# Kernel optimization log

Hardware: AMD Instinct MI355X
Metric: run time of the kernel (lower is better)

The kernel has to match this reference:

```python
import jax, jax.numpy as jnp
import numpy as np

B, L, D = 64, 192, 1024        # batch, tokens (pre_len), in_dim
RES, DIFF, COND = 512, 256, 512
H, DH = 16, 64                 # heads, dim_head; inner = H*DH = 1024
INNER = H * DH
DFF = 4 * D                    # LinearEncoder d_ff
LC = 192                       # cond length


def setup_inputs() -> dict:
    key = jax.random.key(0)
    ks = jax.random.split(key, 16)
    n = lambda k, s, sc=1.0: jax.random.normal(k, s, dtype=jnp.float32) * sc
    return {
        "x": n(ks[0], (B, L, D)),
        "conds": n(ks[1], (B, LC, COND)),
        "diff_emb": n(ks[2], (B, DIFF)),
        "w_diff": n(ks[3], (2 * RES, DIFF), 0.02), "b_diff": jnp.zeros((2 * RES,), jnp.float32),
        "w_cond": n(ks[4], (2 * RES, COND), 0.02), "b_cond": jnp.zeros((2 * RES,), jnp.float32),
        "wq": n(ks[5], (INNER, D), 0.02),
        "wk": n(ks[6], (INNER, 2 * RES), 0.02),
        "wv": n(ks[7], (INNER, 2 * RES), 0.02),
        "wo": n(ks[8], (D, INNER), 0.02), "bo": jnp.zeros((D,), jnp.float32),
        "ln1_g": jnp.ones((D,), jnp.float32), "ln1_b": jnp.zeros((D,), jnp.float32),
        "ln2_g": jnp.ones((D,), jnp.float32), "ln2_b": jnp.zeros((D,), jnp.float32),
        "w_out": n(ks[9], (2 * D, RES), 0.02), "b_out": jnp.zeros((2 * D,), jnp.float32),
        "enc_wv": n(ks[10], (D, D), 0.02), "enc_bv": jnp.zeros((D,), jnp.float32),
        "enc_wo": n(ks[11], (D, D), 0.02), "enc_bo": jnp.zeros((D,), jnp.float32),
        "weight_mat": (jnp.eye(L, dtype=jnp.float32) + jax.random.normal(ks[12], (L, L), dtype=jnp.float32))[None],
        "conv1_w": n(ks[13], (DFF, D), 0.02), "conv1_b": jnp.zeros((DFF,), jnp.float32),
        "conv2_w": n(ks[14], (D, DFF), 0.02), "conv2_b": jnp.zeros((D,), jnp.float32),
        "enc_n1_g": jnp.ones((D,), jnp.float32), "enc_n1_b": jnp.zeros((D,), jnp.float32),
        "enc_n2_g": jnp.ones((D,), jnp.float32), "enc_n2_b": jnp.zeros((D,), jnp.float32),
    }


def _ln(x, g, b):
    m = jnp.mean(x, -1, keepdims=True)
    v = jnp.mean((x - m) ** 2, -1, keepdims=True)
    return (x - m) * jax.lax.rsqrt(v + 1e-5) * g + b


def reference(x, conds, diff_emb, w_diff, b_diff, w_cond, b_cond, wq, wk, wv, wo, bo,
              ln1_g, ln1_b, ln2_g, ln2_b, w_out, b_out, enc_wv, enc_bv, enc_wo, enc_bo,
              weight_mat, conv1_w, conv1_b, conv2_w, conv2_b,
              enc_n1_g, enc_n1_b, enc_n2_g, enc_n2_b):
    res = x
    # diff embedding broadcast-add (permute/unsqueeze in torch == add over token dim)
    x = x + (diff_emb @ w_diff.T + b_diff)[:, None, :]          # [B,L,D]
    # --- LinearEncoder (dropout is identity at inference) ---
    values = x @ enc_wv.T + enc_bv
    A = jax.nn.softplus(weight_mat[0])                          # [L,L]
    A = A / jnp.sum(A, -1, keepdims=True)                       # F.normalize(p=1)
    new_x = jnp.einsum('ij,bjd->bid', A, values)                # token mixing
    x = x + new_x @ enc_wo.T + enc_bo
    x = _ln(x, enc_n1_g, enc_n1_b)
    y = jax.nn.gelu(jnp.einsum('bld,fd->blf', x, conv1_w) + conv1_b, approximate=False)
    y = jnp.einsum('blf,df->bld', y, conv2_w) + conv2_b
    x = _ln(x + y, enc_n2_g, enc_n2_b)
    # --- norm1 + cross attention ---
    x = _ln(x, ln1_g, ln1_b)
    cond = conds @ w_cond.T + b_cond                            # [B,Lc,2*RES]
    b, l = x.shape[0], x.shape[1]
    q = (x @ wq.T).reshape(b, l, H, DH)
    k = (cond @ wk.T).reshape(b, -1, H, DH)
    v = (cond @ wv.T).reshape(b, -1, H, DH)
    scale = DH ** -0.5
    sim = jnp.einsum('bihd,bjhd->bhij', q * scale, k)           # [B,H,L,Lc]
    attn = jax.nn.softmax(sim, axis=-1)
    o = jnp.einsum('bhij,bjhd->bihd', attn, v).reshape(b, l, INNER)
    x = o @ wo.T + bo
    # --- gated residual ---
    x = _ln(x, ln2_g, ln2_b)
    gate, filt = jnp.split(x, 2, axis=2)
    x = jnp.tanh(gate) * jax.nn.sigmoid(filt)                   # [B,L,RES]
    x = x @ w_out.T + b_out                                     # [B,L,2D]
    x = jnp.where(x >= 0, x, 0.4 * x)                           # leaky_relu(0.4)
    out, skip = jnp.split(x, 2, axis=2)
    out = (res + out) / jnp.sqrt(jnp.float32(2.0))
    return out, skip
```

## Files before the change

kernel.cpp:

```cpp
#include <hip/hip_runtime.h>

typedef unsigned short ushort_t;
typedef __attribute__((ext_vector_type(8))) short bf16x8;
typedef __attribute__((ext_vector_type(4))) float f32x4;
typedef __attribute__((ext_vector_type(4))) unsigned short u16x4;

#define DEV __device__ __forceinline__

typedef const __attribute__((address_space(1))) void GV;
typedef __attribute__((address_space(3))) void SV;

DEV void gl_lds16(const ushort_t* g, ushort_t* l) {
    __builtin_amdgcn_global_load_lds((GV*)g, (SV*)l, 16, 0, 0);
}

DEV float bf2f(unsigned short u) {
    union { unsigned u; float f; } c; c.u = ((unsigned)u) << 16; return c.f;
}
DEV unsigned short f2bf(float f) {
    union { float f; unsigned u; } c; c.f = f;
    unsigned u = c.u + 0x7fffu + ((c.u >> 16) & 1u);
    return (unsigned short)(u >> 16);
}

DEV f32x4 mfma32(bf16x8 a, bf16x8 b, f32x4 c) {
    return __builtin_amdgcn_mfma_f32_16x16x32_bf16(a, b, c, 0, 0, 0);
}

__global__ void cvt_kernel(const float* __restrict__ in, ushort_t* __restrict__ out, int n4) {
    for (int i = blockIdx.x * 256 + threadIdx.x; i < n4; i += gridDim.x * 256) {
        f32x4 v = *(const f32x4*)(in + (size_t)i * 4);
        u16x4 o;
        #pragma unroll
        for (int j = 0; j < 4; j++) o[j] = f2bf(v[j]);
        *(u16x4*)(out + (size_t)i * 4) = o;
    }
}

__global__ void anorm_kernel(const float* __restrict__ wm, ushort_t* __restrict__ apad) {
    int row = blockIdx.x;
    int lane = threadIdx.x;
    if (row >= 192) {
        apad[row * 192 + lane] = 0;
        apad[row * 192 + lane + 64] = 0;
        apad[row * 192 + lane + 128] = 0;
        return;
    }
    float x0 = wm[row * 192 + lane];
    float x1 = wm[row * 192 + lane + 64];
    float x2 = wm[row * 192 + lane + 128];
    float s0 = (x0 > 20.f) ? x0 : log1pf(expf(x0));
    float s1 = (x1 > 20.f) ? x1 : log1pf(expf(x1));
    float s2 = (x2 > 20.f) ? x2 : log1pf(expf(x2));
    float t = s0 + s1 + s2;
    #pragma unroll
    for (int m = 1; m < 64; m <<= 1) t += __shfl_xor(t, m);
    float inv = 1.f / t;
    apad[row * 192 + lane]       = f2bf(s0 * inv);
    apad[row * 192 + lane + 64]  = f2bf(s1 * inv);
    apad[row * 192 + lane + 128] = f2bf(s2 * inv);
}

__global__ void diffproj_kernel(const float* __restrict__ emb, const float* __restrict__ w,
                                const float* __restrict__ bias, float* __restrict__ out) {
    int id = blockIdx.x * 256 + threadIdx.x;
    int b = id >> 10, n = id & 1023;
    const float* e = emb + b * 256;
    const float* wr = w + (size_t)n * 256;
    float acc = bias[n];
    for (int k2 = 0; k2 < 256; k2++) acc += e[k2] * wr[k2];
    out[id] = acc;
}

__global__ void x1_kernel(const float* __restrict__ x, const float* __restrict__ dp,
                          ushort_t* __restrict__ out) {
    const size_t N4 = 12288ULL * 1024 / 4;
    for (size_t i = (size_t)blockIdx.x * 256 + threadIdx.x; i < N4; i += (size_t)gridDim.x * 256) {
        size_t e = i * 4;
        size_t row = e >> 10;
        int d = (int)(e & 1023);
        int bb = (int)(row / 192);
        f32x4 xv = *(const f32x4*)(x + e);
        u16x4 o4;
        #pragma unroll
        for (int j = 0; j < 4; j++) o4[j] = f2bf(xv[j] + dp[bb * 1024 + d + j]);
        *(u16x4*)(out + e) = o4;
    }
}

__global__ __launch_bounds__(256) void transp_kernel(const ushort_t* __restrict__ in,
                                                     ushort_t* __restrict__ out) {
    __shared__ ushort_t t[32][33];
    int b = blockIdx.z, jt = blockIdx.y, dt = blockIdx.x;
    int tx = threadIdx.x & 31, ty = threadIdx.x >> 5;
    size_t ib = (size_t)b * 192 * 1024;
    #pragma unroll
    for (int i = 0; i < 4; i++) {
        int j = ty + i * 8;
        t[j][tx] = in[ib + (size_t)(jt * 32 + j) * 1024 + dt * 32 + tx];
    }
    __syncthreads();
    size_t ob = (size_t)b * 1024 * 192;
    #pragma unroll
    for (int i = 0; i < 4; i++) {
        int d = ty + i * 8;
        out[ob + (size_t)(dt * 32 + d) * 192 + jt * 32 + tx] = t[tx][d];
    }
}

template<int EPI>
__global__ __launch_bounds__(256) void gemm_bt(
    const ushort_t* __restrict__ A, int lda, long long sAz,
    const ushort_t* __restrict__ W, int ldw, long long sWz,
    void* __restrict__ Cv, int ldc, long long sCz,
    int Mbound, int K,
    const float* __restrict__ bias,
    const ushort_t* __restrict__ resid,
    float scale,
    const float* __restrict__ resf)
{
    __shared__ ushort_t As[4096];
    __shared__ ushort_t Bs[4096];
    const int tid = threadIdx.x;
    const int wave = tid >> 6, lane = tid & 63, l15 = lane & 15, g = lane >> 4;
    const int wm = wave >> 1, wn = wave & 1;
    const ushort_t* Ab = A + (size_t)blockIdx.z * sAz + (size_t)blockIdx.y * 128 * lda;
    const ushort_t* Wb = W + (size_t)blockIdx.z * sWz + (size_t)blockIdx.x * 128 * ldw;
    const int ob = wave * 1024 + lane * 16;
    const int r0 = ob >> 6, c0 = (ob & 63) >> 1;
    f32x4 acc[4][4] = {};
    for (int k0 = 0; k0 < K; k0 += 32) {
        gl_lds16(Ab + (size_t)r0 * lda + (k0 + c0), As + wave * 512);
        gl_lds16(Ab + (size_t)(r0 + 64) * lda + (k0 + c0), As + 2048 + wave * 512);
        gl_lds16(Wb + (size_t)r0 * ldw + (k0 + c0), Bs + wave * 512);
        gl_lds16(Wb + (size_t)(r0 + 64) * ldw + (k0 + c0), Bs + 2048 + wave * 512);
        __syncthreads();
        bf16x8 af[4], bfr[4];
        const ushort_t* Ar = &As[(wm * 64 + l15) * 32 + g * 8];
        const ushort_t* Br = &Bs[(wn * 64 + l15) * 32 + g * 8];
        #pragma unroll
        for (int i = 0; i < 4; i++) {
            af[i]  = *(const bf16x8*)(Ar + i * 512);
            bfr[i] = *(const bf16x8*)(Br + i * 512);
        }
        #pragma unroll
        for (int mi = 0; mi < 4; mi++)
            #pragma unroll
            for (int ni = 0; ni < 4; ni++)
                acc[mi][ni] = mfma32(af[mi], bfr[ni], acc[mi][ni]);
        __syncthreads();
    }
    const int Rbase = blockIdx.y * 128 + wm * 64;
    const int Cbase = blockIdx.x * 128 + wn * 64;
    #pragma unroll
    for (int mi = 0; mi < 4; mi++) {
        #pragma unroll
        for (int ni = 0; ni < 4; ni++) {
            int Cc = Cbase + ni * 16 + l15;
            float bval = 0.f;
            if (EPI == 1 || EPI == 2 || EPI == 3 || EPI == 5) bval = bias[Cc];
            #pragma unroll
            for (int q = 0; q < 4; q++) {
                int R = Rbase + mi * 16 + g * 4 + q;
                if (R < Mbound) {
                    float t = acc[mi][ni][q];
                    if (EPI == 5) {
                        t += bval;
                        t = (t >= 0.f) ? t : 0.4f * t;
                        float* Of = (float*)Cv;
                        if (Cc < 1024)
                            Of[(size_t)R * 1024 + Cc] = (resf[(size_t)R * 1024 + Cc] + t) * 0.70710678118654752f;
                        else
                            Of[12582912ULL + (size_t)R * 1024 + (Cc - 1024)] = t;
                    } else {
                        ushort_t* Co = (ushort_t*)Cv + (size_t)blockIdx.z * sCz;
                        if (EPI == 1) t += bval;
                        if (EPI == 2) { t += bval; t = 0.5f * t * (1.f + erff(t * 0.70710678118654752f)); }
                        if (EPI == 3) { t += bval + bf2f(resid[(size_t)R * ldc + Cc]); }
                        if (EPI == 4) { t *= scale; }
                        Co[(size_t)R * ldc + Cc] = f2bf(t);
                    }
                }
            }
        }
    }
}

DEV void red2(float& a, float& b) {
    #pragma unroll
    for (int m = 1; m < 64; m <<= 1) { a += __shfl_xor(a, m); b += __shfl_xor(b, m); }
    __shared__ float sa[4], sb[4];
    int w = threadIdx.x >> 6;
    __syncthreads();
    if ((threadIdx.x & 63) == 0) { sa[w] = a; sb[w] = b; }
    __syncthreads();
    a = sa[0] + sa[1] + sa[2] + sa[3];
    b = sb[0] + sb[1] + sb[2] + sb[3];
}

__global__ __launch_bounds__(256) void ln_kernel(const ushort_t* __restrict__ in,
                                                 const float* __restrict__ gg, const float* __restrict__ bb,
                                                 ushort_t* __restrict__ out) {
    size_t row = blockIdx.x;
    int c0 = threadIdx.x * 4;
    u16x4 r4 = *(const u16x4*)(in + row * 1024 + c0);
    float x[4];
    float s = 0.f, sq = 0.f;
    #pragma unroll
    for (int j = 0; j < 4; j++) { x[j] = bf2f(r4[j]); s += x[j]; sq += x[j] * x[j]; }
    red2(s, sq);
    float m = s * (1.f / 1024.f);
    float var = sq * (1.f / 1024.f) - m * m;
    float rs = rsqrtf(var + 1e-5f);
    u16x4 o4;
    #pragma unroll
    for (int j = 0; j < 4; j++) o4[j] = f2bf((x[j] - m) * rs * gg[c0 + j] + bb[c0 + j]);
    *(u16x4*)(out + row * 1024 + c0) = o4;
}

__global__ __launch_bounds__(256) void ln2_kernel(const ushort_t* __restrict__ in,
                                                  const float* __restrict__ g1, const float* __restrict__ b1,
                                                  const float* __restrict__ g2, const float* __restrict__ b2,
                                                  ushort_t* __restrict__ out) {
    size_t row = blockIdx.x;
    int c0 = threadIdx.x * 4;
    u16x4 r4 = *(const u16x4*)(in + row * 1024 + c0);
    float x[4];
    float s = 0.f, sq = 0.f;
    #pragma unroll
    for (int j = 0; j < 4; j++) { x[j] = bf2f(r4[j]); s += x[j]; sq += x[j] * x[j]; }
    red2(s, sq);
    float m = s * (1.f / 1024.f);
    float var = sq * (1.f / 1024.f) - m * m;
    float rs = rsqrtf(var + 1e-5f);
    float t[4];
    float s2 = 0.f, sq2 = 0.f;
    #pragma unroll
    for (int j = 0; j < 4; j++) {
        t[j] = (x[j] - m) * rs * g1[c0 + j] + b1[c0 + j];
        s2 += t[j]; sq2 += t[j] * t[j];
    }
    red2(s2, sq2);
    float m2 = s2 * (1.f / 1024.f);
    float var2 = sq2 * (1.f / 1024.f) - m2 * m2;
    float rs2 = rsqrtf(var2 + 1e-5f);
    u16x4 o4;
    #pragma unroll
    for (int j = 0; j < 4; j++) o4[j] = f2bf((t[j] - m2) * rs2 * g2[c0 + j] + b2[c0 + j]);
    *(u16x4*)(out + row * 1024 + c0) = o4;
}

__global__ __launch_bounds__(256) void lngate_kernel(const ushort_t* __restrict__ in,
                                                     const float* __restrict__ gg, const float* __restrict__ bb,
                                                     ushort_t* __restrict__ out) {
    __shared__ float buf[1024];
    size_t row = blockIdx.x;
    int c0 = threadIdx.x * 4;
    u16x4 r4 = *(const u16x4*)(in + row * 1024 + c0);
    float x[4];
    float s = 0.f, sq = 0.f;
    #pragma unroll
    for (int j = 0; j < 4; j++) { x[j] = bf2f(r4[j]); s += x[j]; sq += x[j] * x[j]; }
    red2(s, sq);
    float m = s * (1.f / 1024.f);
    float var = sq * (1.f / 1024.f) - m * m;
    float rs = rsqrtf(var + 1e-5f);
    #pragma unroll
    for (int j = 0; j < 4; j++) buf[c0 + j] = (x[j] - m) * rs * gg[c0 + j] + bb[c0 + j];
    __syncthreads();
    if (threadIdx.x < 128) {
        int c = threadIdx.x * 4;
        u16x4 o4;
        #pragma unroll
        for (int j = 0; j < 4; j++) {
            float gv = buf[c + j], fv = buf[c + j + 512];
            o4[j] = f2bf(tanhf(gv) * (1.f / (1.f + expf(-fv))));
        }
        *(u16x4*)(out + row * 512 + c) = o4;
    }
}

__global__ __launch_bounds__(256) void attn_kernel(const ushort_t* __restrict__ q,
                                                   const ushort_t* __restrict__ k,
                                                   const ushort_t* __restrict__ v,
                                                   ushort_t* __restrict__ o) {
    __shared__ ushort_t vT[64][208];
    __shared__ ushort_t pS[4][16][208];
    const int tid = threadIdx.x, wave = tid >> 6, lane = tid & 63, l15 = lane & 15, g = lane >> 4;
    const int qb = blockIdx.x, h = blockIdx.y, b = blockIdx.z;
    const size_t base = (size_t)b * 192 * 1024 + h * 64;
    #pragma unroll
    for (int it = 0; it < 6; ++it) {
        int idx = it * 256 + tid;
        int j = idx >> 3, d8 = (idx & 7) * 8;
        bf16x8 vv = *(const bf16x8*)(v + base + (size_t)j * 1024 + d8);
        #pragma unroll
        for (int e = 0; e < 8; e++) vT[d8 + e][j] = (ushort_t)vv[e];
    }
    const int qrow = qb * 64 + wave * 16 + l15;
    bf16x8 aq[2];
    #pragma unroll
    for (int kk = 0; kk < 2; kk++)
        aq[kk] = *(const bf16x8*)(q + base + (size_t)qrow * 1024 + kk * 32 + g * 8);
    f32x4 s[12] = {};
    #pragma unroll
    for (int ni = 0; ni < 12; ni++) {
        #pragma unroll
        for (int kk = 0; kk < 2; kk++) {
            bf16x8 bk = *(const bf16x8*)(k + base + (size_t)(ni * 16 + l15) * 1024 + kk * 32 + g * 8);
            s[ni] = mfma32(aq[kk], bk, s[ni]);
        }
    }
    float sminv[4];
    #pragma unroll
    for (int qq = 0; qq < 4; qq++) {
        float m = s[0][qq];
        #pragma unroll
        for (int ni = 1; ni < 12; ni++) m = fmaxf(m, s[ni][qq]);
        #pragma unroll
        for (int msk = 1; msk < 16; msk <<= 1) m = fmaxf(m, __shfl_xor(m, msk));
        float sum = 0.f;
        #pragma unroll
        for (int ni = 0; ni < 12; ni++) {
            float p = expf(s[ni][qq] - m);
            s[ni][qq] = p;
            sum += p;
        }
        #pragma unroll
        for (int msk = 1; msk < 16; msk <<= 1) sum += __shfl_xor(sum, msk);
        sminv[qq] = 1.f / sum;
    }
    #pragma unroll
    for (int ni = 0; ni < 12; ni++)
        #pragma unroll
        for (int qq = 0; qq < 4; qq++)
            pS[wave][g * 4 + qq][ni * 16 + l15] = f2bf(s[ni][qq]);
    __syncthreads();
    f32x4 oa[4] = {};
    #pragma unroll
    for (int ks = 0; ks < 6; ks++) {
        bf16x8 pa = *(const bf16x8*)(&pS[wave][l15][ks * 32 + g * 8]);
        #pragma unroll
        for (int di = 0; di < 4; di++) {
            bf16x8 bv = *(const bf16x8*)(&vT[di * 16 + l15][ks * 32 + g * 8]);
            oa[di] = mfma32(pa, bv, oa[di]);
        }
    }
    #pragma unroll
    for (int di = 0; di < 4; di++)
        #pragma unroll
        for (int qq = 0; qq < 4; qq++) {
            int row = qb * 64 + wave * 16 + g * 4 + qq;
            o[(size_t)b * 192 * 1024 + (size_t)row * 1024 + h * 64 + di * 16 + l15] =
                f2bf(oa[di][qq] * sminv[qq]);
        }
}

extern "C" void kernel_launch(void* const* d_in, const int* in_sizes, int n_in,
                              void* d_out, int out_size, void* d_ws, size_t ws_size,
                              hipStream_t stream) {
    (void)in_sizes; (void)n_in; (void)out_size; (void)ws_size;
    const float* x_f     = (const float*)d_in[0];
    const float* conds   = (const float*)d_in[1];
    const float* demb    = (const float*)d_in[2];
    const float* w_diff  = (const float*)d_in[3];
    const float* b_diff  = (const float*)d_in[4];
    const float* w_cond  = (const float*)d_in[5];
    const float* b_cond  = (const float*)d_in[6];
    const float* wq      = (const float*)d_in[7];
    const float* wk      = (const float*)d_in[8];
    const float* wv      = (const float*)d_in[9];
    const float* wo      = (const float*)d_in[10];
    const float* bo      = (const float*)d_in[11];
    const float* ln1_g   = (const float*)d_in[12];
    const float* ln1_b   = (const float*)d_in[13];
    const float* ln2_g   = (const float*)d_in[14];
    const float* ln2_b   = (const float*)d_in[15];
    const float* w_out   = (const float*)d_in[16];
    const float* b_out   = (const float*)d_in[17];
    const float* enc_wv  = (const float*)d_in[18];
    const float* enc_bv  = (const float*)d_in[19];
    const float* enc_wo  = (const float*)d_in[20];
    const float* enc_bo  = (const float*)d_in[21];
    const float* wmat    = (const float*)d_in[22];
    const float* conv1_w = (const float*)d_in[23];
    const float* conv1_b = (const float*)d_in[24];
    const float* conv2_w = (const float*)d_in[25];
    const float* conv2_b = (const float*)d_in[26];
    const float* en1_g   = (const float*)d_in[27];
    const float* en1_b   = (const float*)d_in[28];
    const float* en2_g   = (const float*)d_in[29];
    const float* en2_b   = (const float*)d_in[30];

    char* ws = (char*)d_ws;
    size_t off = 0;
    auto nxt = [&](size_t b) { size_t r = off; off += (b + 255) & ~(size_t)255; return r; };

    const size_t RB = 12288ULL * 1024 * 2;
    size_t o_wencv = nxt(1048576 * 2);
    size_t o_wenco = nxt(1048576 * 2);
    size_t o_conv1 = nxt(4194304 * 2);
    size_t o_conv2 = nxt(4194304 * 2);
    size_t o_wq    = nxt(1048576 * 2);
    size_t o_wk    = nxt(1048576 * 2);
    size_t o_wv    = nxt(1048576 * 2);
    size_t o_wo    = nxt(1048576 * 2);
    size_t o_wcond = nxt(524288 * 2);
    size_t o_wout  = nxt(1048576 * 2);
    size_t o_apad  = nxt(256 * 192 * 2);
    size_t o_dp    = nxt(64 * 1024 * 4);
    size_t o_R     = nxt(8 * RB);

    auto WS = [&](size_t o_) { return (ushort_t*)(ws + o_); };
    auto R  = [&](int i)     { return (ushort_t*)(ws + o_R + (size_t)i * RB); };

    auto cvt = [&](const float* src, size_t dst, int n) {
        cvt_kernel<<<dim3(512), dim3(256), 0, stream>>>(src, WS(dst), n / 4);
    };

    cvt(enc_wv, o_wencv, 1048576);
    cvt(enc_wo, o_wenco, 1048576);
    cvt(conv1_w, o_conv1, 4194304);
    cvt(conv2_w, o_conv2, 4194304);
    cvt(wq, o_wq, 1048576);
    cvt(wk, o_wk, 1048576);
    cvt(wv, o_wv, 1048576);
    cvt(wo, o_wo, 1048576);
    cvt(w_cond, o_wcond, 524288);
    cvt(w_out, o_wout, 1048576);

    anorm_kernel<<<dim3(256), dim3(64), 0, stream>>>(wmat, WS(o_apad));
    diffproj_kernel<<<dim3(256), dim3(256), 0, stream>>>(demb, w_diff, b_diff, (float*)(ws + o_dp));
    x1_kernel<<<dim3(3072), dim3(256), 0, stream>>>(x_f, (const float*)(ws + o_dp), R(0));

    gemm_bt<1><<<dim3(8, 96, 1), 256, 0, stream>>>(R(0), 1024, 0, WS(o_wencv), 1024, 0,
        R(1), 1024, 0, 12288, 1024, enc_bv, nullptr, 0.f, nullptr);
    transp_kernel<<<dim3(32, 6, 64), 256, 0, stream>>>(R(1), R(2));
    gemm_bt<0><<<dim3(8, 2, 64), 256, 0, stream>>>(WS(o_apad), 192, 0, R(2), 192, 196608LL,
        R(3), 1024, 196608LL, 192, 192, nullptr, nullptr, 0.f, nullptr);
    gemm_bt<3><<<dim3(8, 96, 1), 256, 0, stream>>>(R(3), 1024, 0, WS(o_wenco), 1024, 0,
        R(4), 1024, 0, 12288, 1024, enc_bo, R(0), 0.f, nullptr);
    ln_kernel<<<dim3(12288), 256, 0, stream>>>(R(4), en1_g, en1_b, R(5));
    gemm_bt<2><<<dim3(32, 96, 1), 256, 0, stream>>>(R(5), 1024, 0, WS(o_conv1), 1024, 0,
        R(0), 4096, 0, 12288, 1024, conv1_b, nullptr, 0.f, nullptr);
    gemm_bt<3><<<dim3(8, 96, 1), 256, 0, stream>>>(R(0), 4096, 0, WS(o_conv2), 4096, 0,
        R(6), 1024, 0, 12288, 4096, conv2_b, R(5), 0.f, nullptr);
    ln2_kernel<<<dim3(12288), 256, 0, stream>>>(R(6), en2_g, en2_b, ln1_g, ln1_b, R(7));
    gemm_bt<4><<<dim3(8, 96, 1), 256, 0, stream>>>(R(7), 1024, 0, WS(o_wq), 1024, 0,
        R(0), 1024, 0, 12288, 1024, nullptr, nullptr, 0.125f, nullptr);
    cvt_kernel<<<dim3(512), dim3(256), 0, stream>>>(conds, R(4), 6291456 / 4);
    gemm_bt<1><<<dim3(8, 96, 1), 256, 0, stream>>>(R(4), 512, 0, WS(o_wcond), 512, 0,
        R(5), 1024, 0, 12288, 512, b_cond, nullptr, 0.f, nullptr);
    gemm_bt<0><<<dim3(8, 96, 1), 256, 0, stream>>>(R(5), 1024, 0, WS(o_wk), 1024, 0,
        R(1), 1024, 0, 12288, 1024, nullptr, nullptr, 0.f, nullptr);
    gemm_bt<0><<<dim3(8, 96, 1), 256, 0, stream>>>(R(5), 1024, 0, WS(o_wv), 1024, 0,
        R(2), 1024, 0, 12288, 1024, nullptr, nullptr, 0.f, nullptr);
    attn_kernel<<<dim3(3, 16, 64), 256, 0, stream>>>(R(0), R(1), R(2), R(3));
    gemm_bt<1><<<dim3(8, 96, 1), 256, 0, stream>>>(R(3), 1024, 0, WS(o_wo), 1024, 0,
        R(6), 1024, 0, 12288, 1024, bo, nullptr, 0.f, nullptr);
    lngate_kernel<<<dim3(12288), 256, 0, stream>>>(R(6), ln2_g, ln2_b, R(4));
    gemm_bt<5><<<dim3(16, 96, 1), 256, 0, stream>>>(R(4), 512, 0, WS(o_wout), 512, 0,
        d_out, 1024, 0, 12288, 512, b_out, nullptr, 0.f, x_f);
}
```

Before: 1.188 ms.

## Replace GEMM with 256x256 double-buffered swizzled kernel and fuse K/V projections

Replaces the 128x128 single-buffered GEMM with a 512-thread kernel using 256x256 output tiles and a BK=64 double-buffered LDS pipeline. The pipeline uses manual vmcnt waits and raw barriers, an XOR-swizzled LDS layout, an XCD-aware block remap and raised wave priority around MFMA bursts. The K and V projection weights are concatenated so one GEMM writes an interleaved KV buffer, and the attention kernel gains a KV stride parameter to read it. The ten weight conversion launches are merged into one multi-segment kernel. The intent is more data reuse per tile, overlap of global loads with MFMA, fewer bank conflicts and fewer launches. In exchange, the 128KB of LDS per block limits occupancy, and the large tiles can leave the small batched M=192 GEMM underutilized.

```diff
diff --git a/kernel.cpp b/kernel.cpp
--- a/kernel.cpp
+++ b/kernel.cpp
@@ -25,6 +25,28 @@
 
 DEV f32x4 mfma32(bf16x8 a, bf16x8 b, f32x4 c) {
     return __builtin_amdgcn_mfma_f32_16x16x32_bf16(a, b, c, 0, 0, 0);
+}
+
+#define VMCNT4  asm volatile("s_waitcnt vmcnt(4)" ::: "memory")
+#define VMCNT8  asm volatile("s_waitcnt vmcnt(8)" ::: "memory")
+#define VMCNT10 asm volatile("s_waitcnt vmcnt(10)" ::: "memory")
+#define VMCNT0  asm volatile("s_waitcnt vmcnt(0)" ::: "memory")
+
+struct CvtSeg { const float* src; ushort_t* dst; };
+struct CvtArgs { CvtSeg s[10]; int cum[11]; };
+
+__global__ void cvt_multi(CvtArgs a, int total4) {
+    for (int i = blockIdx.x * 256 + threadIdx.x; i < total4; i += gridDim.x * 256) {
+        int seg = 0;
+        #pragma unroll
+        for (int t = 1; t < 10; t++) if (i >= a.cum[t]) seg = t;
+        int off = i - a.cum[seg];
+        f32x4 v = *(const f32x4*)(a.s[seg].src + (size_t)off * 4);
+        u16x4 o;
+        #pragma unroll
+        for (int j = 0; j < 4; j++) o[j] = f2bf(v[j]);
+        *(u16x4*)(a.s[seg].dst + (size_t)off * 4) = o;
+    }
 }
 
 __global__ void cvt_kernel(const float* __restrict__ in, ushort_t* __restrict__ out, int n4) {
@@ -109,7 +131,7 @@
 }
 
 template<int EPI>
-__global__ __launch_bounds__(256) void gemm_bt(
+__global__ __launch_bounds__(512, 2) void gemm256(
     const ushort_t* __restrict__ A, int lda, long long sAz,
     const ushort_t* __restrict__ W, int ldw, long long sWz,
     void* __restrict__ Cv, int ldc, long long sCz,
@@ -119,67 +141,131 @@
     float scale,
     const float* __restrict__ resf)
 {
-    __shared__ ushort_t As[4096];
-    __shared__ ushort_t Bs[4096];
+    __shared__ ushort_t smem[65536];
     const int tid = threadIdx.x;
     const int wave = tid >> 6, lane = tid & 63, l15 = lane & 15, g = lane >> 4;
-    const int wm = wave >> 1, wn = wave & 1;
-    const ushort_t* Ab = A + (size_t)blockIdx.z * sAz + (size_t)blockIdx.y * 128 * lda;
-    const ushort_t* Wb = W + (size_t)blockIdx.z * sWz + (size_t)blockIdx.x * 128 * ldw;
-    const int ob = wave * 1024 + lane * 16;
-    const int r0 = ob >> 6, c0 = (ob & 63) >> 1;
-    f32x4 acc[4][4] = {};
-    for (int k0 = 0; k0 < K; k0 += 32) {
-        gl_lds16(Ab + (size_t)r0 * lda + (k0 + c0), As + wave * 512);
-        gl_lds16(Ab + (size_t)(r0 + 64) * lda + (k0 + c0), As + 2048 + wave * 512);
-        gl_lds16(Wb + (size_t)r0 * ldw + (k0 + c0), Bs + wave * 512);
-        gl_lds16(Wb + (size_t)(r0 + 64) * ldw + (k0 + c0), Bs + 2048 + wave * 512);
-        __syncthreads();
-        bf16x8 af[4], bfr[4];
-        const ushort_t* Ar = &As[(wm * 64 + l15) * 32 + g * 8];
-        const ushort_t* Br = &Bs[(wn * 64 + l15) * 32 + g * 8];
-        #pragma unroll
-        for (int i = 0; i < 4; i++) {
-            af[i]  = *(const bf16x8*)(Ar + i * 512);
-            bfr[i] = *(const bf16x8*)(Br + i * 512);
-        }
-        #pragma unroll
-        for (int mi = 0; mi < 4; mi++)
+    const int wm = wave >> 2, wn = wave & 3;
+
+    int bx = blockIdx.x, by = blockIdx.y;
+    if (gridDim.z == 1) {
+        int gx = gridDim.x, nwg = gx * gridDim.y;
+        if ((nwg & 7) == 0) {
+            int orig = by * gx + bx;
+            int logi = (orig & 7) * (nwg >> 3) + (orig >> 3);
+            bx = logi % gx; by = logi / gx;
+        }
+    }
+    const ushort_t* Ab = A + (size_t)blockIdx.z * sAz + (size_t)by * 256 * lda;
+    const ushort_t* Wb = W + (size_t)blockIdx.z * sWz + (size_t)bx * 256 * ldw;
+
+    const int rsub  = lane >> 3;
+    const int swsrc = ((lane & 7) ^ (lane >> 3)) * 8;
+    const int NT = K >> 6;
+
+    auto STAGE = [&](int kt, int buf) {
+        const int k0 = kt << 6;
+        ushort_t* AL = smem + buf * 16384;
+        ushort_t* BL = smem + 32768 + buf * 16384;
+        gl_lds16(Ab + (size_t)((wave     ) * 8 + rsub) * lda + k0 + swsrc, AL + (wave     ) * 512);
+        gl_lds16(Ab + (size_t)((wave +  8) * 8 + rsub) * lda + k0 + swsrc, AL + (wave +  8) * 512);
+        gl_lds16(Wb + (size_t)((wave     ) * 8 + rsub) * ldw + k0 + swsrc, BL + (wave     ) * 512);
+        gl_lds16(Wb + (size_t)((wave +  8) * 8 + rsub) * ldw + k0 + swsrc, BL + (wave +  8) * 512);
+        gl_lds16(Wb + (size_t)((wave + 16) * 8 + rsub) * ldw + k0 + swsrc, BL + (wave + 16) * 512);
+        gl_lds16(Wb + (size_t)((wave + 24) * 8 + rsub) * ldw + k0 + swsrc, BL + (wave + 24) * 512);
+        gl_lds16(Ab + (size_t)((wave + 16) * 8 + rsub) * lda + k0 + swsrc, AL + (wave + 16) * 512);
+        gl_lds16(Ab + (size_t)((wave + 24) * 8 + rsub) * lda + k0 + swsrc, AL + (wave + 24) * 512);
+    };
+
+    auto LDA = [&](bf16x8 (&aa)[4][2], int mh, int buf) {
+        const char* base = (const char*)smem + buf * 32768;
+        #pragma unroll
+        for (int m = 0; m < 4; m++) {
+            int r = mh * 128 + wm * 64 + m * 16 + l15;
             #pragma unroll
-            for (int ni = 0; ni < 4; ni++)
-                acc[mi][ni] = mfma32(af[mi], bfr[ni], acc[mi][ni]);
-        __syncthreads();
-    }
-    const int Rbase = blockIdx.y * 128 + wm * 64;
-    const int Cbase = blockIdx.x * 128 + wn * 64;
-    #pragma unroll
-    for (int mi = 0; mi < 4; mi++) {
-        #pragma unroll
-        for (int ni = 0; ni < 4; ni++) {
-            int Cc = Cbase + ni * 16 + l15;
-            float bval = 0.f;
-            if (EPI == 1 || EPI == 2 || EPI == 3 || EPI == 5) bval = bias[Cc];
+            for (int kk = 0; kk < 2; kk++) {
+                int byo = r * 128 + ((kk * 64 + g * 16) ^ ((l15 & 7) << 4));
+                aa[m][kk] = *(const bf16x8*)(base + byo);
+            }
+        }
+    };
+    auto LDB = [&](bf16x8 (&bb)[2][2], int nh, int buf) {
+        const char* base = (const char*)smem + 65536 + buf * 32768;
+        #pragma unroll
+        for (int n = 0; n < 2; n++) {
+            int r = nh * 128 + wn * 32 + n * 16 + l15;
             #pragma unroll
-            for (int q = 0; q < 4; q++) {
-                int R = Rbase + mi * 16 + g * 4 + q;
-                if (R < Mbound) {
-                    float t = acc[mi][ni][q];
-                    if (EPI == 5) {
-                        t += bval;
-                        t = (t >= 0.f) ? t : 0.4f * t;
-                        float* Of = (float*)Cv;
-                        if (Cc < 1024)
-                            Of[(size_t)R * 1024 + Cc] = (resf[(size_t)R * 1024 + Cc] + t) * 0.70710678118654752f;
-                        else
-                            Of[12582912ULL + (size_t)R * 1024 + (Cc - 1024)] = t;
-                    } else {
-                        ushort_t* Co = (ushort_t*)Cv + (size_t)blockIdx.z * sCz;
-                        if (EPI == 1) t += bval;
-                        if (EPI == 2) { t += bval; t = 0.5f * t * (1.f + erff(t * 0.70710678118654752f)); }
-                        if (EPI == 3) { t += bval + bf2f(resid[(size_t)R * ldc + Cc]); }
-                        if (EPI == 4) { t *= scale; }
-                        Co[(size_t)R * ldc + Cc] = f2bf(t);
-                    }
+            for (int kk = 0; kk < 2; kk++) {
+                int byo = r * 128 + ((kk * 64 + g * 16) ^ ((l15 & 7) << 4));
+                bb[n][kk] = *(const bf16x8*)(base + byo);
+            }
+        }
+    };
+
+    f32x4 acc[2][2][4][2] = {};
+    bf16x8 afr[4][2], bfr[2][2];
+
+    auto MM = [&](f32x4 (&aq)[4][2]) {
+        __builtin_amdgcn_s_setprio(1);
+        #pragma unroll
+        for (int m = 0; m < 4; m++)
+            #pragma unroll
+            for (int n = 0; n < 2; n++)
+                #pragma unroll
+                for (int kk = 0; kk < 2; kk++)
+                    aq[m][n] = mfma32(afr[m][kk], bfr[n][kk], aq[m][n]);
+        __builtin_amdgcn_s_setprio(0);
+    };
+
+    STAGE(0, 0);
+    for (int kt = 0; kt < NT; kt++) {
+        const int buf = kt & 1;
+        const int ktn = (kt + 1 < NT) ? kt + 1 : NT - 1;
+        VMCNT4; __builtin_amdgcn_s_barrier();
+        LDA(afr, 0, buf); LDB(bfr, 0, buf);
+        STAGE(ktn, buf ^ 1);
+        MM(acc[0][0]);
+        VMCNT10; __builtin_amdgcn_s_barrier();
+        LDB(bfr, 1, buf);
+        MM(acc[0][1]);
+        VMCNT8; __builtin_amdgcn_s_barrier();
+        LDA(afr, 1, buf);
+        MM(acc[1][1]);
+        LDB(bfr, 0, buf);
+        MM(acc[1][0]);
+    }
+    VMCNT0;
+
+    #pragma unroll
+    for (int mh = 0; mh < 2; mh++)
+    #pragma unroll
+    for (int nh = 0; nh < 2; nh++)
+    #pragma unroll
+    for (int m = 0; m < 4; m++)
+    #pragma unroll
+    for (int n = 0; n < 2; n++) {
+        int Cc = bx * 256 + nh * 128 + wn * 32 + n * 16 + l15;
+        float bval = 0.f;
+        if (EPI == 1 || EPI == 2 || EPI == 3 || EPI == 5) bval = bias[Cc];
+        #pragma unroll
+        for (int q = 0; q < 4; q++) {
+            int R = by * 256 + mh * 128 + wm * 64 + m * 16 + g * 4 + q;
+            if (R < Mbound) {
+                float t = acc[mh][nh][m][n][q];
+                if (EPI == 5) {
+                    t += bval;
+                    t = (t >= 0.f) ? t : 0.4f * t;
+                    float* Of = (float*)Cv;
+                    if (Cc < 1024)
+                        Of[(size_t)R * 1024 + Cc] = (resf[(size_t)R * 1024 + Cc] + t) * 0.70710678118654752f;
+                    else
+                        Of[12582912ULL + (size_t)R * 1024 + (Cc - 1024)] = t;
+                } else {
+                    ushort_t* Co = (ushort_t*)Cv + (size_t)blockIdx.z * sCz;
+                    if (EPI == 1) t += bval;
+                    if (EPI == 2) { t += bval; t = 0.5f * t * (1.f + erff(t * 0.70710678118654752f)); }
+                    if (EPI == 3) { t += bval + bf2f(resid[(size_t)R * ldc + Cc]); }
+                    if (EPI == 4) { t *= scale; }
+                    Co[(size_t)R * ldc + Cc] = f2bf(t);
                 }
             }
         }
@@ -283,17 +369,18 @@
 __global__ __launch_bounds__(256) void attn_kernel(const ushort_t* __restrict__ q,
                                                    const ushort_t* __restrict__ k,
                                                    const ushort_t* __restrict__ v,
-                                                   ushort_t* __restrict__ o) {
+                                                   ushort_t* __restrict__ o, int ldkv) {
     __shared__ ushort_t vT[64][208];
     __shared__ ushort_t pS[4][16][208];
     const int tid = threadIdx.x, wave = tid >> 6, lane = tid & 63, l15 = lane & 15, g = lane >> 4;
     const int qb = blockIdx.x, h = blockIdx.y, b = blockIdx.z;
-    const size_t base = (size_t)b * 192 * 1024 + h * 64;
+    const size_t baseq = (size_t)b * 192 * 1024 + h * 64;
+    const size_t basekv = (size_t)b * 192 * ldkv + h * 64;
     #pragma unroll
     for (int it = 0; it < 6; ++it) {
         int idx = it * 256 + tid;
         int j = idx >> 3, d8 = (idx & 7) * 8;
-        bf16x8 vv = *(const bf16x8*)(v + base + (size_t)j * 1024 + d8);
+        bf16x8 vv = *(const bf16x8*)(v + basekv + (size_t)j * ldkv + d8);
         #pragma unroll
         for (int e = 0; e < 8; e++) vT[d8 + e][j] = (ushort_t)vv[e];
     }
@@ -301,13 +388,13 @@
     bf16x8 aq[2];
     #pragma unroll
     for (int kk = 0; kk < 2; kk++)
-        aq[kk] = *(const bf16x8*)(q + base + (size_t)qrow * 1024 + kk * 32 + g * 8);
+        aq[kk] = *(const bf16x8*)(q + baseq + (size_t)qrow * 1024 + kk * 32 + g * 8);
     f32x4 s[12] = {};
     #pragma unroll
     for (int ni = 0; ni < 12; ni++) {
         #pragma unroll
         for (int kk = 0; kk < 2; kk++) {
-            bf16x8 bk = *(const bf16x8*)(k + base + (size_t)(ni * 16 + l15) * 1024 + kk * 32 + g * 8);
+            bf16x8 bk = *(const bf16x8*)(k + basekv + (size_t)(ni * 16 + l15) * ldkv + kk * 32 + g * 8);
             s[ni] = mfma32(aq[kk], bk, s[ni]);
         }
     }
@@ -402,8 +489,7 @@
     size_t o_conv1 = nxt(4194304 * 2);
     size_t o_conv2 = nxt(4194304 * 2);
     size_t o_wq    = nxt(1048576 * 2);
-    size_t o_wk    = nxt(1048576 * 2);
-    size_t o_wv    = nxt(1048576 * 2);
+    size_t o_wkv   = nxt(2097152 * 2);
     size_t o_wo    = nxt(1048576 * 2);
     size_t o_wcond = nxt(524288 * 2);
     size_t o_wout  = nxt(1048576 * 2);
@@ -414,51 +500,47 @@
     auto WS = [&](size_t o_) { return (ushort_t*)(ws + o_); };
     auto R  = [&](int i)     { return (ushort_t*)(ws + o_R + (size_t)i * RB); };
 
-    auto cvt = [&](const float* src, size_t dst, int n) {
-        cvt_kernel<<<dim3(512), dim3(256), 0, stream>>>(src, WS(dst), n / 4);
-    };
-
-    cvt(enc_wv, o_wencv, 1048576);
-    cvt(enc_wo, o_wenco, 1048576);
-    cvt(conv1_w, o_conv1, 4194304);
-    cvt(conv2_w, o_conv2, 4194304);
-    cvt(wq, o_wq, 1048576);
-    cvt(wk, o_wk, 1048576);
-    cvt(wv, o_wv, 1048576);
-    cvt(wo, o_wo, 1048576);
-    cvt(w_cond, o_wcond, 524288);
-    cvt(w_out, o_wout, 1048576);
+    {
+        CvtArgs ca;
+        const float* srcs[10] = { enc_wv, enc_wo, conv1_w, conv2_w, wq, wk, wv, wo, w_cond, w_out };
+        ushort_t*    dsts[10] = { WS(o_wencv), WS(o_wenco), WS(o_conv1), WS(o_conv2), WS(o_wq),
+                                  WS(o_wkv), WS(o_wkv) + 1048576, WS(o_wo), WS(o_wcond), WS(o_wout) };
+        int          n4s[10]  = { 262144, 262144, 1048576, 1048576, 262144,
+                                  262144, 262144, 262144, 131072, 262144 };
+        int cum = 0;
+        for (int i = 0; i < 10; i++) { ca.s[i].src = srcs[i]; ca.s[i].dst = dsts[i]; ca.cum[i] = cum; cum += n4s[i]; }
+        ca.cum[10] = cum;
+        cvt_multi<<<dim3(1024), dim3(256), 0, stream>>>(ca, cum);
+    }
 
     anorm_kernel<<<dim3(256), dim3(64), 0, stream>>>(wmat, WS(o_apad));
     diffproj_kernel<<<dim3(256), dim3(256), 0, stream>>>(demb, w_diff, b_diff, (float*)(ws + o_dp));
     x1_kernel<<<dim3(3072), dim3(256), 0, stream>>>(x_f, (const float*)(ws + o_dp), R(0));
 
-    gemm_bt<1><<<dim3(8, 96, 1), 256, 0, stream>>>(R(0), 1024, 0, WS(o_wencv), 1024, 0,
+    gemm256<1><<<dim3(4, 48, 1), 512, 0, stream>>>(R(0), 1024, 0, WS(o_wencv), 1024, 0,
         R(1), 1024, 0, 12288, 1024, enc_bv, nullptr, 0.f, nullptr);
     transp_kernel<<<dim3(32, 6, 64), 256, 0, stream>>>(R(1), R(2));
-    gemm_bt<0><<<dim3(8, 2, 64), 256, 0, stream>>>(WS(o_apad), 192, 0, R(2), 192, 196608LL,
+    gemm256<0><<<dim3(4, 1, 64), 512, 0, stream>>>(WS(o_apad), 192, 0, R(2), 192, 196608LL,
         R(3), 1024, 196608LL, 192, 192, nullptr, nullptr, 0.f, nullptr);
-    gemm_bt<3><<<dim3(8, 96, 1), 256, 0, stream>>>(R(3), 1024, 0, WS(o_wenco), 1024, 0,
+    gemm256<3><<<dim3(4, 48, 1), 512, 0, stream>>>(R(3), 1024, 0, WS(o_wenco), 1024, 0,
         R(4), 1024, 0, 12288, 1024, enc_bo, R(0), 0.f, nullptr);
     ln_kernel<<<dim3(12288), 256, 0, stream>>>(R(4), en1_g, en1_b, R(5));
-    gemm_bt<2><<<dim3(32, 96, 1), 256, 0, stream>>>(R(5), 1024, 0, WS(o_conv1), 1024, 0,
+    gemm256<2><<<dim3(16, 48, 1), 512, 0, stream>>>(R(5), 1024, 0, WS(o_conv1), 1024, 0,
         R(0), 4096, 0, 12288, 1024, conv1_b, nullptr, 0.f, nullptr);
-    gemm_bt<3><<<dim3(8, 96, 1), 256, 0, stream>>>(R(0), 4096, 0, WS(o_conv2), 4096, 0,
+    gemm256<3><<<dim3(4, 48, 1), 512, 0, stream>>>(R(0), 4096, 0, WS(o_conv2), 4096, 0,
         R(6), 1024, 0, 12288, 4096, conv2_b, R(5), 0.f, nullptr);
     ln2_kernel<<<dim3(12288), 256, 0, stream>>>(R(6), en2_g, en2_b, ln1_g, ln1_b, R(7));
-    gemm_bt<4><<<dim3(8, 96, 1), 256, 0, stream>>>(R(7), 1024, 0, WS(o_wq), 1024, 0,
+    gemm256<4><<<dim3(4, 48, 1), 512, 0, stream>>>(R(7), 1024, 0, WS(o_wq), 1024, 0,
         R(0), 1024, 0, 12288, 1024, nullptr, nullptr, 0.125f, nullptr);
     cvt_kernel<<<dim3(512), dim3(256), 0, stream>>>(conds, R(4), 6291456 / 4);
-    gemm_bt<1><<<dim3(8, 96, 1), 256, 0, stream>>>(R(4), 512, 0, WS(o_wcond), 512, 0,
+    gemm256<1><<<dim3(4, 48, 1), 512, 0, stream>>>(R(4), 512, 0, WS(o_wcond), 512, 0,
         R(5), 1024, 0, 12288, 512, b_cond, nullptr, 0.f, nullptr);
-    gemm_bt<0><<<dim3(8, 96, 1), 256, 0, stream>>>(R(5), 1024, 0, WS(o_wk), 1024, 0,
-        R(1), 1024, 0, 12288, 1024, nullptr, nullptr, 0.f, nullptr);
-    gemm_bt<0><<<dim3(8, 96, 1), 256, 0, stream>>>(R(5), 1024, 0, WS(o_wv), 1024, 0,
-        R(2), 1024, 0, 12288, 1024, nullptr, nullptr, 0.f, nullptr);
-    attn_kernel<<<dim3(3, 16, 64), 256, 0, stream>>>(R(0), R(1), R(2), R(3));
-    gemm_bt<1><<<dim3(8, 96, 1), 256, 0, stream>>>(R(3), 1024, 0, WS(o_wo), 1024, 0,
+    gemm256<0><<<dim3(8, 48, 1), 512, 0, stream>>>(R(5), 1024, 0, WS(o_wkv), 1024, 0,
+        R(1), 2048, 0, 12288, 1024, nullptr, nullptr, 0.f, nullptr);
+    attn_kernel<<<dim3(3, 16, 64), 256, 0, stream>>>(R(0), R(1), R(1) + 1024, R(3), 2048);
+    gemm256<1><<<dim3(4, 48, 1), 512, 0, stream>>>(R(3), 1024, 0, WS(o_wo), 1024, 0,
         R(6), 1024, 0, 12288, 1024, bo, nullptr, 0.f, nullptr);
     lngate_kernel<<<dim3(12288), 256, 0, stream>>>(R(6), ln2_g, ln2_b, R(4));
-    gemm_bt<5><<<dim3(16, 96, 1), 256, 0, stream>>>(R(4), 512, 0, WS(o_wout), 512, 0,
+    gemm256<5><<<dim3(8, 48, 1), 512, 0, stream>>>(R(4), 512, 0, WS(o_wout), 512, 0,
         d_out, 1024, 0, 12288, 512, b_out, nullptr, 0.f, x_f);
 }
```

Measured after the change: 1.151 ms. 1.03x faster.
